# Optimization experiments

Hardware: AMD Instinct MI355X
Metric: run time of the kernel (lower is better)

The kernel has to match this reference:

```python
import jax, jax.numpy as jnp
import numpy as np

B, T, H = 4096, 1024, 15


def setup_inputs() -> dict:
    key = jax.random.key(0)
    ks = jax.random.split(key, 7)
    return {
        "x": jax.random.normal(ks[0], (B, T, 1), dtype=jnp.float32),
        "w_ih": jax.random.normal(ks[1], (H, 1), dtype=jnp.float32) * (1.0 / np.sqrt(H)),
        "w_hh": jax.random.normal(ks[2], (H, H), dtype=jnp.float32) * (1.0 / np.sqrt(H)),
        "b_ih": jax.random.normal(ks[3], (H,), dtype=jnp.float32) * (1.0 / np.sqrt(H)),
        "b_hh": jax.random.normal(ks[4], (H,), dtype=jnp.float32) * (1.0 / np.sqrt(H)),
        "w_lin": jax.random.normal(ks[5], (1, H), dtype=jnp.float32) * (1.0 / np.sqrt(H)),
        "b_lin": jax.random.normal(ks[6], (1,), dtype=jnp.float32) * (1.0 / np.sqrt(H)),
    }


def reference(x, w_ih, w_hh, b_ih, b_hh, w_lin, b_lin):
    # Single-layer tanh RNN (batch_first), then per-timestep linear head.
    # Precompute the input projection for all timesteps: [B, T, H]
    xp = jnp.einsum("bti,hi->bth", x, w_ih) + b_ih + b_hh
    xp_t = jnp.swapaxes(xp, 0, 1)  # [T, B, H] for scan over time

    def step(h, xt):
        # h: [B, H], xt: [B, H]
        h_new = jnp.tanh(xt + h @ w_hh.T)
        return h_new, h_new

    h0 = jnp.zeros((x.shape[0], w_hh.shape[0]), dtype=x.dtype)
    _, hs = jax.lax.scan(step, h0, xp_t)  # hs: [T, B, H]
    hs = jnp.swapaxes(hs, 0, 1)  # [B, T, H]
    return jnp.einsum("bth,oh->bto", hs, w_lin) + b_lin  # [B, T, 1]
```

## Files before the change

### kernel.cpp

```cpp
#include <hip/hip_runtime.h>

#define B_ 4096
#define T_ 1024
#define H_ 15

#define STEP(XT, ODST)                                                        \
  do {                                                                        \
    float base_ = fmaf((XT), wih2, bias2);                                    \
    float cA_, cB_, cC_, cD_, e_;                                             \
    asm("s_nop 1\n\t"                                                         \
        "v_mul_f32_dpp %[cA], %[u], %[w1] row_ror:1 row_mask:0xf bank_mask:0xf\n\t"  \
        "v_mul_f32_dpp %[cB], %[u], %[w2] row_ror:2 row_mask:0xf bank_mask:0xf\n\t"  \
        "v_mul_f32_dpp %[cC], %[u], %[w3] row_ror:3 row_mask:0xf bank_mask:0xf\n\t"  \
        "v_fma_f32 %[cD], %[u], %[w0], %[bs]\n\t"                             \
        "v_add_f32_dpp %[pp], %[pp], %[pp] row_shr:1 row_mask:0xf bank_mask:0xf\n\t" \
        "v_fmac_f32_dpp %[cA], %[u], %[w5] row_ror:5 row_mask:0xf bank_mask:0xf\n\t" \
        "v_fmac_f32_dpp %[cB], %[u], %[w6] row_ror:6 row_mask:0xf bank_mask:0xf\n\t" \
        "v_add_f32_dpp %[pp], %[pp], %[pp] row_shr:2 row_mask:0xf bank_mask:0xf\n\t" \
        "v_fmac_f32_dpp %[cC], %[u], %[w7] row_ror:7 row_mask:0xf bank_mask:0xf\n\t" \
        "v_fmac_f32_dpp %[cD], %[u], %[w4] row_ror:4 row_mask:0xf bank_mask:0xf\n\t" \
        "v_add_f32_dpp %[pp], %[pp], %[pp] row_shr:4 row_mask:0xf bank_mask:0xf\n\t" \
        "v_fmac_f32_dpp %[cA], %[u], %[w9] row_ror:9 row_mask:0xf bank_mask:0xf\n\t" \
        "v_fmac_f32_dpp %[cB], %[u], %[w10] row_ror:10 row_mask:0xf bank_mask:0xf\n\t" \
        "v_add_f32_dpp %[pp], %[pp], %[pp] row_shr:8 row_mask:0xf bank_mask:0xf\n\t" \
        "v_fmac_f32_dpp %[cC], %[u], %[w11] row_ror:11 row_mask:0xf bank_mask:0xf\n\t" \
        "v_fmac_f32_dpp %[cD], %[u], %[w8] row_ror:8 row_mask:0xf bank_mask:0xf\n\t"  \
        "v_add_f32 %[o], %[pp], %[Cc]\n\t"                                    \
        "v_fmac_f32_dpp %[cA], %[u], %[w13] row_ror:13 row_mask:0xf bank_mask:0xf\n\t" \
        "v_fmac_f32_dpp %[cB], %[u], %[w14] row_ror:14 row_mask:0xf bank_mask:0xf\n\t" \
        "v_fmac_f32_dpp %[cC], %[u], %[w15] row_ror:15 row_mask:0xf bank_mask:0xf\n\t" \
        "v_fmac_f32_dpp %[cD], %[u], %[w12] row_ror:12 row_mask:0xf bank_mask:0xf\n\t" \
        "v_add_f32 %[cA], %[cA], %[cB]\n\t"                                   \
        "v_add_f32 %[cC], %[cC], %[cD]\n\t"                                   \
        "v_add_f32 %[cA], %[cA], %[cC]\n\t"                                   \
        "v_exp_f32 %[e], %[cA]\n\t"                                           \
        "s_nop 0\n\t"                                                         \
        "v_add_f32 %[e], 1.0, %[e]\n\t"                                       \
        "v_rcp_f32 %[u], %[e]\n\t"                                            \
        "s_nop 0\n\t"                                                         \
        "v_mul_f32 %[pp], %[u], %[wl]\n\t"                                    \
        : [u] "+v"(u), [pp] "+v"(pp), [o] "=&v"(ODST), [cA] "=&v"(cA_),       \
          [cB] "=&v"(cB_), [cC] "=&v"(cC_), [cD] "=&v"(cD_), [e] "=&v"(e_)    \
        : [bs] "v"(base_), [wl] "v"(wl2), [Cc] "v"(C),                        \
          [w0] "v"(wr[0]), [w1] "v"(wr[1]), [w2] "v"(wr[2]),                  \
          [w3] "v"(wr[3]), [w4] "v"(wr[4]), [w5] "v"(wr[5]),                  \
          [w6] "v"(wr[6]), [w7] "v"(wr[7]), [w8] "v"(wr[8]),                  \
          [w9] "v"(wr[9]), [w10] "v"(wr[10]), [w11] "v"(wr[11]),              \
          [w12] "v"(wr[12]), [w13] "v"(wr[13]), [w14] "v"(wr[14]),            \
          [w15] "v"(wr[15]));                                                 \
  } while (0)

#define ADD_SHR_EPI(p, n)                                                     \
  do {                                                                        \
    float _t;                                                                 \
    asm("s_nop 1\n\tv_add_f32_dpp %0, %1, %1 row_shr:" #n                     \
        " row_mask:0xf bank_mask:0xf"                                         \
        : "=v"(_t) : "v"(p));                                                 \
    p = _t;                                                                   \
  } while (0)

#define POS(K, XV)                                                            \
  do {                                                                        \
    float o_;                                                                 \
    STEP(XV, o_);                                                             \
    osta[((K) + 3) & 3] = o_;                                                 \
    if (((K) & 3) == 0) {                                                     \
      if ((K) > 0 || t > 0) {                                                 \
        if (m == 15)                                                          \
          *(float4*)(ob + t + (K) - 4) =                                      \
              make_float4(osta[0], osta[1], osta[2], osta[3]);                \
      }                                                                       \
    }                                                                         \
    if (((K) & 3) == 3) {                                                     \
      int _tn = t + 32 + (((K) >> 2) << 2);                                   \
      if (_tn >= T_) _tn = 0;          \
      qq[(K) >> 2] = *(const float4*)(xb + _tn);                              \
    }                                                                         \
  } while (0)

__global__ __attribute__((amdgpu_flat_work_group_size(256, 256),
                          amdgpu_waves_per_eu(1, 1)))
void rnn_tanh_kernel(
    const float* __restrict__ x, const float* __restrict__ w_ih,
    const float* __restrict__ w_hh, const float* __restrict__ b_ih,
    const float* __restrict__ b_hh, const float* __restrict__ w_lin,
    const float* __restrict__ b_lin, float* __restrict__ out) {
  const int tid = threadIdx.x;
  const int m = tid & 15;
  const int b = blockIdx.x * 16 + (tid >> 4);

  const float S = 2.8853900817779268f;

  float wr[16];
#pragma unroll
  for (int n = 0; n < 16; ++n) {
    const int c = (m - n) & 15;
    wr[n] = (m < H_ && c < H_) ? -2.0f * S * w_hh[m * H_ + c] : 0.0f;
  }
  float rowsum = 0.0f;
  if (m < H_)
    for (int j = 0; j < H_; ++j) rowsum += w_hh[m * H_ + j];
  const float wih2  = (m < H_) ? S * w_ih[m] : 0.0f;
  const float bias2 = (m < H_) ? S * (b_ih[m] + b_hh[m] + rowsum) : 0.0f;
  const float wl2   = (m < H_) ? -2.0f * w_lin[m] : 0.0f;
  float wsum = b_lin[0];
  for (int j = 0; j < H_; ++j) wsum += w_lin[j];
  const float C = wsum;

  const float* xb = x + (size_t)b * T_;
  float* ob = out + (size_t)b * T_;

  float u = 0.5f;
  float pp = u * wl2;
  float osta[4];

  float4 qq[8];
#pragma unroll
  for (int j = 0; j < 8; ++j) qq[j] = *(const float4*)(xb + 4 * j);

  for (int t = 0; t < T_; t += 32) {
    POS(0,  qq[0].x); POS(1,  qq[0].y); POS(2,  qq[0].z); POS(3,  qq[0].w);
    POS(4,  qq[1].x); POS(5,  qq[1].y); POS(6,  qq[1].z); POS(7,  qq[1].w);
    POS(8,  qq[2].x); POS(9,  qq[2].y); POS(10, qq[2].z); POS(11, qq[2].w);
    POS(12, qq[3].x); POS(13, qq[3].y); POS(14, qq[3].z); POS(15, qq[3].w);
    POS(16, qq[4].x); POS(17, qq[4].y); POS(18, qq[4].z); POS(19, qq[4].w);
    POS(20, qq[5].x); POS(21, qq[5].y); POS(22, qq[5].z); POS(23, qq[5].w);
    POS(24, qq[6].x); POS(25, qq[6].y); POS(26, qq[6].z); POS(27, qq[6].w);
    POS(28, qq[7].x); POS(29, qq[7].y); POS(30, qq[7].z); POS(31, qq[7].w);
  }

  ADD_SHR_EPI(pp, 1);
  ADD_SHR_EPI(pp, 2);
  ADD_SHR_EPI(pp, 4);
  ADD_SHR_EPI(pp, 8);
  osta[3] = pp + C;
  if (m == 15)
    *(float4*)(ob + T_ - 4) = make_float4(osta[0], osta[1], osta[2], osta[3]);
}

extern "C" void kernel_launch(void* const* d_in, const int* in_sizes, int n_in,
                              void* d_out, int out_size, void* d_ws, size_t ws_size,
                              hipStream_t stream) {
  (void)in_sizes; (void)n_in; (void)out_size; (void)d_ws; (void)ws_size;
  rnn_tanh_kernel<<<B_ / 16, 256, 0, stream>>>(
      (const float*)d_in[0], (const float*)d_in[1], (const float*)d_in[2],
      (const float*)d_in[3], (const float*)d_in[4], (const float*)d_in[5],
      (const float*)d_in[6], (float*)d_out);
}
```

Baseline: 154.4 us.

## Compute linear head in idle 16th lane via the recurrence matvec

The per-step output projection used to be a separate DPP shift-add reduction of u*w_lin. It now runs in the otherwise unused lane 15 of each 16-lane row: that lane's weight row holds -2*w_lin and its bias holds C, so the same rotated-FMA matvec produces the output. This removes four dependent DPP adds and a multiply per step, and the x-projection FMA moves into the asm block. The cost is that lane 15 also runs exp/rcp on its value, which is harmless, and the output now comes from the matvec accumulator before the tanh.

```diff
diff --git a/kernel.cpp b/kernel.cpp
--- a/kernel.cpp
+++ b/kernel.cpp
@@ -6,57 +6,41 @@
 
 #define STEP(XT, ODST)                                                        \
   do {                                                                        \
-    float base_ = fmaf((XT), wih2, bias2);                                    \
-    float cA_, cB_, cC_, cD_, e_;                                             \
-    asm("s_nop 1\n\t"                                                         \
-        "v_mul_f32_dpp %[cA], %[u], %[w1] row_ror:1 row_mask:0xf bank_mask:0xf\n\t"  \
-        "v_mul_f32_dpp %[cB], %[u], %[w2] row_ror:2 row_mask:0xf bank_mask:0xf\n\t"  \
-        "v_mul_f32_dpp %[cC], %[u], %[w3] row_ror:3 row_mask:0xf bank_mask:0xf\n\t"  \
+    float bs_, cB_, cC_, cD_, e_;                                             \
+    asm("v_fma_f32 %[bs], %[xt], %[wih], %[bias]\n\t"                         \
+        "v_mul_f32_dpp %[acc], %[u], %[w1] row_ror:1 row_mask:0xf bank_mask:0xf\n\t"  \
+        "v_mul_f32_dpp %[cB], %[u], %[w2] row_ror:2 row_mask:0xf bank_mask:0xf\n\t"   \
+        "v_mul_f32_dpp %[cC], %[u], %[w3] row_ror:3 row_mask:0xf bank_mask:0xf\n\t"   \
         "v_fma_f32 %[cD], %[u], %[w0], %[bs]\n\t"                             \
-        "v_add_f32_dpp %[pp], %[pp], %[pp] row_shr:1 row_mask:0xf bank_mask:0xf\n\t" \
-        "v_fmac_f32_dpp %[cA], %[u], %[w5] row_ror:5 row_mask:0xf bank_mask:0xf\n\t" \
-        "v_fmac_f32_dpp %[cB], %[u], %[w6] row_ror:6 row_mask:0xf bank_mask:0xf\n\t" \
-        "v_add_f32_dpp %[pp], %[pp], %[pp] row_shr:2 row_mask:0xf bank_mask:0xf\n\t" \
-        "v_fmac_f32_dpp %[cC], %[u], %[w7] row_ror:7 row_mask:0xf bank_mask:0xf\n\t" \
-        "v_fmac_f32_dpp %[cD], %[u], %[w4] row_ror:4 row_mask:0xf bank_mask:0xf\n\t" \
-        "v_add_f32_dpp %[pp], %[pp], %[pp] row_shr:4 row_mask:0xf bank_mask:0xf\n\t" \
-        "v_fmac_f32_dpp %[cA], %[u], %[w9] row_ror:9 row_mask:0xf bank_mask:0xf\n\t" \
+        "v_fmac_f32_dpp %[acc], %[u], %[w5] row_ror:5 row_mask:0xf bank_mask:0xf\n\t" \
+        "v_fmac_f32_dpp %[cB], %[u], %[w6] row_ror:6 row_mask:0xf bank_mask:0xf\n\t"  \
+        "v_fmac_f32_dpp %[cC], %[u], %[w7] row_ror:7 row_mask:0xf bank_mask:0xf\n\t"  \
+        "v_fmac_f32_dpp %[cD], %[u], %[w4] row_ror:4 row_mask:0xf bank_mask:0xf\n\t"  \
+        "v_fmac_f32_dpp %[acc], %[u], %[w9] row_ror:9 row_mask:0xf bank_mask:0xf\n\t" \
         "v_fmac_f32_dpp %[cB], %[u], %[w10] row_ror:10 row_mask:0xf bank_mask:0xf\n\t" \
-        "v_add_f32_dpp %[pp], %[pp], %[pp] row_shr:8 row_mask:0xf bank_mask:0xf\n\t" \
         "v_fmac_f32_dpp %[cC], %[u], %[w11] row_ror:11 row_mask:0xf bank_mask:0xf\n\t" \
         "v_fmac_f32_dpp %[cD], %[u], %[w8] row_ror:8 row_mask:0xf bank_mask:0xf\n\t"  \
-        "v_add_f32 %[o], %[pp], %[Cc]\n\t"                                    \
-        "v_fmac_f32_dpp %[cA], %[u], %[w13] row_ror:13 row_mask:0xf bank_mask:0xf\n\t" \
+        "v_fmac_f32_dpp %[acc], %[u], %[w13] row_ror:13 row_mask:0xf bank_mask:0xf\n\t" \
         "v_fmac_f32_dpp %[cB], %[u], %[w14] row_ror:14 row_mask:0xf bank_mask:0xf\n\t" \
         "v_fmac_f32_dpp %[cC], %[u], %[w15] row_ror:15 row_mask:0xf bank_mask:0xf\n\t" \
         "v_fmac_f32_dpp %[cD], %[u], %[w12] row_ror:12 row_mask:0xf bank_mask:0xf\n\t" \
-        "v_add_f32 %[cA], %[cA], %[cB]\n\t"                                   \
+        "v_add_f32 %[acc], %[acc], %[cB]\n\t"                                 \
         "v_add_f32 %[cC], %[cC], %[cD]\n\t"                                   \
-        "v_add_f32 %[cA], %[cA], %[cC]\n\t"                                   \
-        "v_exp_f32 %[e], %[cA]\n\t"                                           \
+        "v_add_f32 %[acc], %[acc], %[cC]\n\t"                                 \
+        "v_exp_f32 %[e], %[acc]\n\t"                                          \
         "s_nop 0\n\t"                                                         \
         "v_add_f32 %[e], 1.0, %[e]\n\t"                                       \
         "v_rcp_f32 %[u], %[e]\n\t"                                            \
         "s_nop 0\n\t"                                                         \
-        "v_mul_f32 %[pp], %[u], %[wl]\n\t"                                    \
-        : [u] "+v"(u), [pp] "+v"(pp), [o] "=&v"(ODST), [cA] "=&v"(cA_),       \
-          [cB] "=&v"(cB_), [cC] "=&v"(cC_), [cD] "=&v"(cD_), [e] "=&v"(e_)    \
-        : [bs] "v"(base_), [wl] "v"(wl2), [Cc] "v"(C),                        \
+        : [u] "+v"(u), [acc] "=&v"(ODST), [bs] "=&v"(bs_), [cB] "=&v"(cB_),   \
+          [cC] "=&v"(cC_), [cD] "=&v"(cD_), [e] "=&v"(e_)                     \
+        : [xt] "v"(XT), [wih] "v"(wih2), [bias] "v"(bias2),                   \
           [w0] "v"(wr[0]), [w1] "v"(wr[1]), [w2] "v"(wr[2]),                  \
           [w3] "v"(wr[3]), [w4] "v"(wr[4]), [w5] "v"(wr[5]),                  \
           [w6] "v"(wr[6]), [w7] "v"(wr[7]), [w8] "v"(wr[8]),                  \
           [w9] "v"(wr[9]), [w10] "v"(wr[10]), [w11] "v"(wr[11]),              \
           [w12] "v"(wr[12]), [w13] "v"(wr[13]), [w14] "v"(wr[14]),            \
           [w15] "v"(wr[15]));                                                 \
-  } while (0)
-
-#define ADD_SHR_EPI(p, n)                                                     \
-  do {                                                                        \
-    float _t;                                                                 \
-    asm("s_nop 1\n\tv_add_f32_dpp %0, %1, %1 row_shr:" #n                     \
-        " row_mask:0xf bank_mask:0xf"                                         \
-        : "=v"(_t) : "v"(p));                                                 \
-    p = _t;                                                                   \
   } while (0)
 
 #define POS(K, XV)                                                            \
@@ -91,27 +75,30 @@
 
   const float S = 2.8853900817779268f;
 
+  float wsum = b_lin[0];
+  for (int j = 0; j < H_; ++j) wsum += w_lin[j];
+  const float C = wsum;
+
   float wr[16];
 #pragma unroll
   for (int n = 0; n < 16; ++n) {
     const int c = (m - n) & 15;
-    wr[n] = (m < H_ && c < H_) ? -2.0f * S * w_hh[m * H_ + c] : 0.0f;
+    if (m < H_)
+      wr[n] = (c < H_) ? -2.0f * S * w_hh[m * H_ + c] : 0.0f;
+    else
+      wr[n] = (c < H_) ? -2.0f * w_lin[c] : 0.0f;
   }
   float rowsum = 0.0f;
   if (m < H_)
     for (int j = 0; j < H_; ++j) rowsum += w_hh[m * H_ + j];
   const float wih2  = (m < H_) ? S * w_ih[m] : 0.0f;
-  const float bias2 = (m < H_) ? S * (b_ih[m] + b_hh[m] + rowsum) : 0.0f;
-  const float wl2   = (m < H_) ? -2.0f * w_lin[m] : 0.0f;
-  float wsum = b_lin[0];
-  for (int j = 0; j < H_; ++j) wsum += w_lin[j];
-  const float C = wsum;
+  const float bias2 = (m < H_) ? S * (b_ih[m] + b_hh[m] + rowsum) : C;
 
   const float* xb = x + (size_t)b * T_;
   float* ob = out + (size_t)b * T_;
 
   float u = 0.5f;
-  float pp = u * wl2;
+  asm("s_nop 1" : "+v"(u));
   float osta[4];
 
   float4 qq[8];
@@ -129,13 +116,13 @@
     POS(28, qq[7].x); POS(29, qq[7].y); POS(30, qq[7].z); POS(31, qq[7].w);
   }
 
-  ADD_SHR_EPI(pp, 1);
-  ADD_SHR_EPI(pp, 2);
-  ADD_SHR_EPI(pp, 4);
-  ADD_SHR_EPI(pp, 8);
-  osta[3] = pp + C;
-  if (m == 15)
-    *(float4*)(ob + T_ - 4) = make_float4(osta[0], osta[1], osta[2], osta[3]);
+  {
+    float o_;
+    STEP(0.0f, o_);
+    osta[3] = o_;
+    if (m == 15)
+      *(float4*)(ob + T_ - 4) = make_float4(osta[0], osta[1], osta[2], osta[3]);
+  }
 }
 
 extern "C" void kernel_launch(void* const* d_in, const int* in_sizes, int n_in,
```

Result: faster. 141.7 us (-8.3%).
